# Performance work log

Measured on AMD Instinct MI355X. Metric: run time of the kernel, lower is better.

The kernel has to match this reference:

```python
import jax, jax.numpy as jnp
import numpy as np

B, S, H = 32, 2048, 1024

def setup_inputs() -> dict:
    key = jax.random.key(0)
    k1, k2, k3, k4, k5 = jax.random.split(key, 5)
    hidden = jax.random.normal(k1, (1, B, H), dtype=jnp.float32)
    encoder_outputs = jax.random.normal(k2, (B, S, H), dtype=jnp.float32)
    # nn.Linear(2H, H): weight [H, 2H], bias [H]
    W_attn = jax.random.normal(k3, (H, 2 * H), dtype=jnp.float32) * (1.0 / np.sqrt(2 * H))
    b_attn = jax.random.normal(k4, (H,), dtype=jnp.float32) * 0.01
    # nn.Linear(H, 1, bias=False): weight [1, H] -> stored as [H]
    v = jax.random.normal(k5, (H,), dtype=jnp.float32) * (1.0 / np.sqrt(H))
    return {"hidden": hidden, "encoder_outputs": encoder_outputs,
            "W_attn": W_attn, "b_attn": b_attn, "v": v}

def reference(hidden, encoder_outputs, W_attn, b_attn, v):
    # hidden: [1, B, H] -> [B, H]; encoder_outputs: [B, S, H]
    h = hidden[0]  # [B, H]
    # cat((hidden_repeated, enc), -1) @ W_attn.T == h @ Wh.T + enc @ We.T
    Wh = W_attn[:, :H]   # [H, H] acts on hidden part
    We = W_attn[:, H:]   # [H, H] acts on encoder part
    h_proj = jnp.einsum('bh,oh->bo', h, Wh)                    # [B, H]
    e_proj = jnp.einsum('bsh,oh->bso', encoder_outputs, We)    # [B, S, H]
    energy = jnp.tanh(e_proj + h_proj[:, None, :] + b_attn)    # [B, S, H]
    attention = jnp.einsum('bsh,h->bs', energy, v)             # [B, S]
    return jax.nn.softmax(attention, axis=1)
```

## Files before the change

kernel.cpp:

```cpp
#include <hip/hip_runtime.h>
#include <hip/hip_bf16.h>
#include <cstdint>


#define HDIM 1024
#define SDIM 2048
#define MTOT 65536

typedef __attribute__((ext_vector_type(8))) short short8;
typedef __attribute__((ext_vector_type(4))) float floatx4;

__device__ __forceinline__ unsigned short f2bf(float f) {
    unsigned int u = __float_as_uint(f);
    u += 0x7fffu + ((u >> 16) & 1u);
    return (unsigned short)(u >> 16);
}
__device__ __forceinline__ unsigned int pack2(float a, float b) {
    return (unsigned int)f2bf(a) | ((unsigned int)f2bf(b) << 16);
}
__device__ __forceinline__ float fast_tanh(float x) {
    float e2 = __expf(2.f * x);
    return 1.f - 2.f * __builtin_amdgcn_rcpf(e2 + 1.f);
}

__global__ __launch_bounds__(256) void prep(const float* __restrict__ W,
                                            unsigned short* __restrict__ Wbf2,
                                            const float* __restrict__ hid,
                                            const float* __restrict__ bias,
                                            float* __restrict__ c) {
    __shared__ float red[4][32];
    if (blockIdx.x < 512) {
        int T = blockIdx.x * 256 + threadIdx.x;
        int n  = T >> 7;
        int k8 = T & 127;
        int k  = k8 * 8;
        const float4* src = (const float4*)(W + (size_t)n * 2048 + 1024 + k);
        float4 f0 = src[0], f1 = src[1];
        int jt = n >> 4, lc = n & 15, kc = k8 >> 2, g = k8 & 3;
        uint4 u;
        u.x = pack2(f0.x, f0.y); u.y = pack2(f0.z, f0.w);
        u.z = pack2(f1.x, f1.y); u.w = pack2(f1.z, f1.w);
        *(uint4*)(Wbf2 + (size_t)(jt * 32 + kc) * 512 + (g * 16 + lc) * 8) = u;
    } else {
        const int o = blockIdx.x - 512;
        const int wave = threadIdx.x >> 6, lane = threadIdx.x & 63;
        const int k = wave * 256 + lane * 4;
        const float4 wv = *(const float4*)(W + (size_t)o * 2048 + k);
        float acc[32];
#pragma unroll
        for (int b = 0; b < 32; ++b) {
            const float4 h = *(const float4*)(hid + b * HDIM + k);
            acc[b] = wv.x * h.x + wv.y * h.y + wv.z * h.z + wv.w * h.w;
        }
#pragma unroll
        for (int b = 0; b < 32; ++b) {
            float x = acc[b];
            for (int off = 32; off; off >>= 1) x += __shfl_xor(x, off);
            if (lane == 0) red[wave][b] = x;
        }
        __syncthreads();
        if (threadIdx.x < 32) {
            int b = threadIdx.x;
            c[b * HDIM + o] = red[0][b] + red[1][b] + red[2][b] + red[3][b] + bias[o];
        }
    }
}

#define PHN 8
#define PHK 128

__global__ __launch_bounds__(512, 2) void attn_fused(const float* __restrict__ enc,
                                                     const unsigned short* __restrict__ Wbf2,
                                                     const float* __restrict__ c,
                                                     const float* __restrict__ v,
                                                     float* __restrict__ part) {
    __shared__ __align__(16) unsigned short slab[2][128 * 128];

    const int tid  = threadIdx.x;
    const int lane = tid & 63;
    const int wave = tid >> 6;
    const int grp  = lane >> 4;
    const int lc   = lane & 15;

    const int strip = blockIdx.x >> 1;
    const int nhalf = blockIdx.x & 1;
    const int m0 = strip * 128;
    const int b  = m0 >> 11;
    const int cb = nhalf * 512 + wave * 64;

    const int s_kk   = (lane & 31) * 4;
    const int s_rsub = lane >> 5;
    const int s_c16  = (lane & 31) >> 1;
    const int s_b8   = lane & 1;

    floatx4 acc[8][4];
#pragma unroll
    for (int i = 0; i < 8; ++i)
#pragma unroll
        for (int j = 0; j < 4; ++j) acc[i][j] = (floatx4){0.f, 0.f, 0.f, 0.f};

    const short8* Bfr = (const short8*)Wbf2;
    const int jt0 = nhalf * 32 + wave * 4;

    float4 ld[8];
#pragma unroll
    for (int q = 0; q < 8; ++q) {
        int row = wave * 16 + q * 2 + s_rsub;
        ld[q] = *(const float4*)(enc + (size_t)(m0 + row) * HDIM + s_kk);
    }
#pragma unroll
    for (int q = 0; q < 8; ++q) {
        int row  = wave * 16 + q * 2 + s_rsub;
        int slot = s_c16 ^ (row & 7);
        uint2 u = {pack2(ld[q].x, ld[q].y), pack2(ld[q].z, ld[q].w)};
        *(uint2*)(&slab[0][row * 128 + slot * 8 + s_b8 * 4]) = u;
    }

    short8 bf[4], bn[4];
#pragma unroll
    for (int j = 0; j < 4; ++j)
        bf[j] = Bfr[(size_t)((jt0 + j) * 32 + 0) * 64 + lane];

#pragma unroll 1
    for (int p = 0; p < PHN; ++p) {
        __syncthreads();

        if (p < PHN - 1) {
#pragma unroll
            for (int q = 0; q < 8; ++q) {
                int row = wave * 16 + q * 2 + s_rsub;
                ld[q] = *(const float4*)(enc + (size_t)(m0 + row) * HDIM +
                                         (p + 1) * PHK + s_kk);
            }
        }

        const unsigned short* sl = slab[p & 1];
#pragma unroll
        for (int s = 0; s < 4; ++s) {
            const int kc = s;
            short8 af[8];
#pragma unroll
            for (int i = 0; i < 8; ++i) {
                int row  = i * 16 + lc;
                int slot = (kc * 4 + grp) ^ (lc & 7);
                af[i] = *(const short8*)(sl + row * 128 + slot * 8);
            }
            {
                const int kc2 = (s + 1) & 3;
                const int pn  = (s < 3) ? p : ((p < PHN - 1) ? p + 1 : p);
#pragma unroll
                for (int j = 0; j < 4; ++j)
                    bn[j] = Bfr[(size_t)((jt0 + j) * 32 + pn * 4 + kc2) * 64 + lane];
            }
#pragma unroll
            for (int i = 0; i < 8; ++i)
#pragma unroll
                for (int j = 0; j < 4; ++j)
                    acc[i][j] = __builtin_amdgcn_mfma_f32_16x16x32_bf16(
                        af[i], bf[j], acc[i][j], 0, 0, 0);
#pragma unroll
            for (int j = 0; j < 4; ++j) bf[j] = bn[j];
        }

        if (p < PHN - 1) {
#pragma unroll
            for (int q = 0; q < 8; ++q) {
                int row  = wave * 16 + q * 2 + s_rsub;
                int slot = s_c16 ^ (row & 7);
                uint2 u = {pack2(ld[q].x, ld[q].y), pack2(ld[q].z, ld[q].w)};
                *(uint2*)(&slab[(p + 1) & 1][row * 128 + slot * 8 + s_b8 * 4]) = u;
            }
        }
    }

    float rowsum[8][4];
#pragma unroll
    for (int i = 0; i < 8; ++i)
#pragma unroll
        for (int r = 0; r < 4; ++r) rowsum[i][r] = 0.f;

#pragma unroll
    for (int j = 0; j < 4; ++j) {
        const int n  = cb + j * 16 + lc;
        const float vn = v[n];
        const float cv = c[b * HDIM + n];
#pragma unroll
        for (int i = 0; i < 8; ++i)
#pragma unroll
            for (int r = 0; r < 4; ++r)
                rowsum[i][r] = fmaf(fast_tanh(acc[i][j][r] + cv), vn,
                                    rowsum[i][r]);
    }

    __syncthreads();
    float* red = (float*)slab;
#pragma unroll
    for (int i = 0; i < 8; ++i)
#pragma unroll
        for (int r = 0; r < 4; ++r) {
            float x = rowsum[i][r];
            x += __shfl_xor(x, 8);
            x += __shfl_xor(x, 4);
            x += __shfl_xor(x, 2);
            x += __shfl_xor(x, 1);
            if (lc == 0) red[wave * 128 + i * 16 + grp * 4 + r] = x;
        }
    __syncthreads();
    if (tid < 128) {
        float ssum = 0.f;
#pragma unroll
        for (int w = 0; w < 8; ++w) ssum += red[w * 128 + tid];
        part[(size_t)nhalf * MTOT + m0 + tid] = ssum;
    }
}

__global__ __launch_bounds__(256) void softmax_k(const float* __restrict__ part,
                                                 float* __restrict__ out) {
    __shared__ float wred[4];
    const int bb = blockIdx.x;
    const int tid = threadIdx.x;
    const int wave = tid >> 6, lane = tid & 63;

    float vals[8];
    float lmax = -INFINITY;
#pragma unroll
    for (int q = 0; q < 8; ++q) {
        const size_t idx = (size_t)bb * SDIM + q * 256 + tid;
        vals[q] = part[idx] + part[(size_t)MTOT + idx];
        lmax = fmaxf(lmax, vals[q]);
    }
    for (int off = 32; off; off >>= 1) lmax = fmaxf(lmax, __shfl_xor(lmax, off));
    if (lane == 0) wred[wave] = lmax;
    __syncthreads();
    lmax = fmaxf(fmaxf(wred[0], wred[1]), fmaxf(wred[2], wred[3]));
    __syncthreads();

    float e[8];
    float s = 0.f;
#pragma unroll
    for (int q = 0; q < 8; ++q) {
        e[q] = __expf(vals[q] - lmax);
        s += e[q];
    }
    for (int off = 32; off; off >>= 1) s += __shfl_xor(s, off);
    if (lane == 0) wred[wave] = s;
    __syncthreads();
    s = wred[0] + wred[1] + wred[2] + wred[3];
    const float inv = 1.f / s;
#pragma unroll
    for (int q = 0; q < 8; ++q)
        out[(size_t)bb * SDIM + q * 256 + tid] = e[q] * inv;
}

extern "C" void kernel_launch(void* const* d_in, const int* in_sizes, int n_in,
                              void* d_out, int out_size, void* d_ws, size_t ws_size,
                              hipStream_t stream) {
    const float* hidden = (const float*)d_in[0];
    const float* enc    = (const float*)d_in[1];
    const float* W      = (const float*)d_in[2];
    const float* battn  = (const float*)d_in[3];
    const float* v      = (const float*)d_in[4];
    float* out = (float*)d_out;

    char* ws = (char*)d_ws;
    float* c             = (float*)ws;
    float* part          = (float*)(ws + (128 << 10));
    unsigned short* Wbf2 = (unsigned short*)(ws + (640 << 10));

    hipLaunchKernelGGL(prep,       dim3(1536), dim3(256), 0, stream, W, Wbf2, hidden, battn, c);
    hipLaunchKernelGGL(attn_fused, dim3(1024), dim3(512), 0, stream, enc, Wbf2, c, v, part);
    hipLaunchKernelGGL(softmax_k,  dim3(32),   dim3(256), 0, stream, part, out);
}
```

Measured before the change: 491.9 us.

## Remap block order for L2 locality, use intrinsic bf16 pack, issue B loads earlier

Block indices are remapped so that consecutive blocks spread strips across XCDs and the two N-halves of a strip land near each other, aiming to improve L2 reuse of encoder rows. The hand-rolled float-to-bf16 rounding is replaced by the HIP __float22bfloat162_rn intrinsic, which may lower to a packed hardware convert. The prefetch of the next B fragments is moved ahead of the LDS A reads to hide global latency. The new mapping assumes a specific grid size (512 strips x 2).

```diff
diff --git a/kernel.cpp b/kernel.cpp
--- a/kernel.cpp
+++ b/kernel.cpp
@@ -10,13 +10,11 @@
 typedef __attribute__((ext_vector_type(8))) short short8;
 typedef __attribute__((ext_vector_type(4))) float floatx4;
 
-__device__ __forceinline__ unsigned short f2bf(float f) {
-    unsigned int u = __float_as_uint(f);
-    u += 0x7fffu + ((u >> 16) & 1u);
-    return (unsigned short)(u >> 16);
-}
 __device__ __forceinline__ unsigned int pack2(float a, float b) {
-    return (unsigned int)f2bf(a) | ((unsigned int)f2bf(b) << 16);
+    __hip_bfloat162 h = __float22bfloat162_rn(float2{a, b});
+    union { __hip_bfloat162 h; unsigned int u; } cv;
+    cv.h = h;
+    return cv.u;
 }
 __device__ __forceinline__ float fast_tanh(float x) {
     float e2 = __expf(2.f * x);
@@ -82,8 +80,9 @@
     const int grp  = lane >> 4;
     const int lc   = lane & 15;
 
-    const int strip = blockIdx.x >> 1;
-    const int nhalf = blockIdx.x & 1;
+    const int j     = blockIdx.x;
+    const int strip = (j & 7) * 64 + (j >> 4);
+    const int nhalf = (j >> 3) & 1;
     const int m0 = strip * 128;
     const int b  = m0 >> 11;
     const int cb = nhalf * 512 + wave * 64;
@@ -97,7 +96,7 @@
 #pragma unroll
     for (int i = 0; i < 8; ++i)
 #pragma unroll
-        for (int j = 0; j < 4; ++j) acc[i][j] = (floatx4){0.f, 0.f, 0.f, 0.f};
+        for (int jj = 0; jj < 4; ++jj) acc[i][jj] = (floatx4){0.f, 0.f, 0.f, 0.f};
 
     const short8* Bfr = (const short8*)Wbf2;
     const int jt0 = nhalf * 32 + wave * 4;
@@ -118,8 +117,8 @@
 
     short8 bf[4], bn[4];
 #pragma unroll
-    for (int j = 0; j < 4; ++j)
-        bf[j] = Bfr[(size_t)((jt0 + j) * 32 + 0) * 64 + lane];
+    for (int jj = 0; jj < 4; ++jj)
+        bf[jj] = Bfr[(size_t)((jt0 + jj) * 32 + 0) * 64 + lane];
 
 #pragma unroll 1
     for (int p = 0; p < PHN; ++p) {
@@ -138,6 +137,13 @@
 #pragma unroll
         for (int s = 0; s < 4; ++s) {
             const int kc = s;
+            {
+                const int kc2 = (s + 1) & 3;
+                const int pn  = (s < 3) ? p : ((p < PHN - 1) ? p + 1 : p);
+#pragma unroll
+                for (int jj = 0; jj < 4; ++jj)
+                    bn[jj] = Bfr[(size_t)((jt0 + jj) * 32 + pn * 4 + kc2) * 64 + lane];
+            }
             short8 af[8];
 #pragma unroll
             for (int i = 0; i < 8; ++i) {
@@ -145,21 +151,14 @@
                 int slot = (kc * 4 + grp) ^ (lc & 7);
                 af[i] = *(const short8*)(sl + row * 128 + slot * 8);
             }
-            {
-                const int kc2 = (s + 1) & 3;
-                const int pn  = (s < 3) ? p : ((p < PHN - 1) ? p + 1 : p);
-#pragma unroll
-                for (int j = 0; j < 4; ++j)
-                    bn[j] = Bfr[(size_t)((jt0 + j) * 32 + pn * 4 + kc2) * 64 + lane];
-            }
 #pragma unroll
             for (int i = 0; i < 8; ++i)
 #pragma unroll
-                for (int j = 0; j < 4; ++j)
-                    acc[i][j] = __builtin_amdgcn_mfma_f32_16x16x32_bf16(
-                        af[i], bf[j], acc[i][j], 0, 0, 0);
-#pragma unroll
-            for (int j = 0; j < 4; ++j) bf[j] = bn[j];
+                for (int jj = 0; jj < 4; ++jj)
+                    acc[i][jj] = __builtin_amdgcn_mfma_f32_16x16x32_bf16(
+                        af[i], bf[jj], acc[i][jj], 0, 0, 0);
+#pragma unroll
+            for (int jj = 0; jj < 4; ++jj) bf[jj] = bn[jj];
         }
 
         if (p < PHN - 1) {
@@ -180,15 +179,15 @@
         for (int r = 0; r < 4; ++r) rowsum[i][r] = 0.f;
 
 #pragma unroll
-    for (int j = 0; j < 4; ++j) {
-        const int n  = cb + j * 16 + lc;
+    for (int jj = 0; jj < 4; ++jj) {
+        const int n  = cb + jj * 16 + lc;
         const float vn = v[n];
         const float cv = c[b * HDIM + n];
 #pragma unroll
         for (int i = 0; i < 8; ++i)
 #pragma unroll
             for (int r = 0; r < 4; ++r)
-                rowsum[i][r] = fmaf(fast_tanh(acc[i][j][r] + cv), vn,
+                rowsum[i][r] = fmaf(fast_tanh(acc[i][jj][r] + cv), vn,
                                     rowsum[i][r]);
     }
 
```

Result: no change. 486.2 us (-1.2%).
